# Performance work log

Measured on AMD Instinct MI355X. Metric: run time of the kernel, lower is better.

## Reference

```python
import jax, jax.numpy as jnp
import numpy as np

EMBED_DIM = 1024
HEADS = 16
HEAD_DIM = EMBED_DIM // HEADS
DIST_LAMBDA = -0.1
LN_EPS = 1e-5


def setup_inputs() -> dict:
    key = jax.random.key(0)
    ks = jax.random.split(key, 16)
    B, N, D = 32, 4096, EMBED_DIM
    s = 1.0 / np.sqrt(D)
    inp = {
        "query": jax.random.normal(ks[0], (B, D), jnp.float32),
        "context": jax.random.normal(ks[1], (B, N, D), jnp.float32),
        "dist_matrix": jax.random.uniform(ks[2], (B, 1, N), jnp.float32),
        "context_mask": jax.random.randint(ks[3], (B, N), 0, 2, jnp.int32),
        "Wq": jax.random.normal(ks[4], (D, D), jnp.float32) * s,
        "bq": jnp.zeros((D,), jnp.float32),
        "Wk": jax.random.normal(ks[5], (D, D), jnp.float32) * s,
        "bk": jnp.zeros((D,), jnp.float32),
        "Wv": jax.random.normal(ks[6], (D, D), jnp.float32) * s,
        "bv": jnp.zeros((D,), jnp.float32),
        "Wo": jax.random.normal(ks[7], (D, D), jnp.float32) * s,
        "bo": jnp.zeros((D,), jnp.float32),
        "ln_gamma": jnp.ones((D,), jnp.float32),
        "ln_beta": jnp.zeros((D,), jnp.float32),
    }
    return inp


def reference(query, context, dist_matrix, context_mask,
              Wq, bq, Wk, bk, Wv, bv, Wo, bo, ln_gamma, ln_beta):
    B, N, D = context.shape
    H, hd = HEADS, HEAD_DIM
    # projections
    q = (query @ Wq + bq).reshape(B, H, hd)            # [B,H,hd] (single query)
    k = (context @ Wk + bk).reshape(B, N, H, hd)       # [B,N,H,hd]
    v = (context @ Wv + bv).reshape(B, N, H, hd)
    # scores: [B,H,N]
    scores = jnp.einsum("bhd,bnhd->bhn", q, k) / np.sqrt(hd)
    # additive Manhattan-distance bias, broadcast over heads
    scores = scores + dist_matrix * DIST_LAMBDA        # dist_matrix [B,1,N]
    # mask
    scores = jnp.where(context_mask[:, None, :] == 0, -1e9, scores)
    attn = jax.nn.softmax(scores, axis=-1)             # [B,H,N]
    attn_out = jnp.einsum("bhn,bnhd->bhd", attn, v).reshape(B, D)
    output = attn_out @ Wo + bo
    x = query + output
    # LayerNorm
    mu = jnp.mean(x, axis=-1, keepdims=True)
    var = jnp.mean((x - mu) ** 2, axis=-1, keepdims=True)
    return (x - mu) * jax.lax.rsqrt(var + LN_EPS) * ln_gamma + ln_beta
```

## Files before the change

### kernel.cpp

```cpp
#include <hip/hip_runtime.h>
#include <hip/hip_bf16.h>
#include <math.h>

#define DDIM 1024
#define NH 16
#define HDIM 64
#define SCALE 0.125f
#define DLAM -0.1f
#define LNEPS 1e-5f
#define NS 16
#define CHW 16
#define BROW 256
#define CBSTR 1032

typedef short bf16x8 __attribute__((ext_vector_type(8)));
typedef float f32x4 __attribute__((ext_vector_type(4)));

__device__ inline unsigned short f2bf(float x) {
    return __builtin_bit_cast(unsigned short, __float2bfloat16(x));
}

__device__ inline void wg_barrier_lds() {
    asm volatile("s_waitcnt lgkmcnt(0)" ::: "memory");
    __builtin_amdgcn_s_barrier();
    __builtin_amdgcn_sched_barrier(0);
}

__global__ __launch_bounds__(512) void k_q(const float* __restrict__ query,
                                           const float* __restrict__ Wq,
                                           const float* __restrict__ bq,
                                           float* __restrict__ qout) {
    int b = blockIdx.x, c0 = blockIdx.y * 128;
    __shared__ float qs[DDIM];
    __shared__ float ps[512];
    int t = threadIdx.x;
    for (int i = t; i < DDIM; i += 512) qs[i] = query[b * DDIM + i];
    __syncthreads();
    int cl = t & 127;
    int col = c0 + cl;
    int d0 = (t >> 7) * 256;
    float acc = 0.f;
#pragma unroll 8
    for (int d = d0; d < d0 + 256; ++d)
        acc = fmaf(qs[d], Wq[(size_t)d * DDIM + col], acc);
    ps[t] = acc;
    __syncthreads();
    if (t < 128)
        qout[b * DDIM + col] = ps[t] + ps[t + 128] + ps[t + 256] + ps[t + 384] + bq[col];
}

__global__ __launch_bounds__(256) void k_qp(const float* __restrict__ qin,
                                            const float* __restrict__ Wk,
                                            unsigned short* __restrict__ qpb) {
    int dt = blockIdx.x, bg = blockIdx.y;
    __shared__ float qs[8][DDIM];
    for (int i = threadIdx.x; i < 8 * DDIM; i += 256)
        qs[i >> 10][i & 1023] =
            qin[(size_t)(bg * 8 + (i >> 10)) * DDIM + (i & 1023)];
    __syncthreads();
    int h = threadIdx.x & 15, dl = threadIdx.x >> 4;
    int d = dt * 16 + dl;
    const float* wr = Wk + (size_t)d * DDIM + h * HDIM;
    float acc[8] = {0.f, 0.f, 0.f, 0.f, 0.f, 0.f, 0.f, 0.f};
#pragma unroll
    for (int j = 0; j < HDIM; ++j) {
        float wv = wr[j];
#pragma unroll
        for (int bb = 0; bb < 8; ++bb)
            acc[bb] = fmaf(wv, qs[bb][h * HDIM + j], acc[bb]);
    }
#pragma unroll
    for (int bb = 0; bb < 8; ++bb)
        qpb[((size_t)((bg * 8 + bb) * NH + h)) * DDIM + d] = f2bf(acc[bb] * SCALE);
}

__global__ __launch_bounds__(512) void k_sb(const float* __restrict__ qin,
                                            const float* __restrict__ bk,
                                            float* __restrict__ sb) {
    int idx = threadIdx.x;
    int b = idx >> 4, h = idx & 15;
    float acc = 0.f;
#pragma unroll
    for (int j = 0; j < HDIM; ++j)
        acc = fmaf(bk[h * HDIM + j], qin[b * DDIM + h * HDIM + j], acc);
    sb[idx] = acc * SCALE;
}

__global__ __launch_bounds__(256, 2) void k_flash2(
    const float* __restrict__ ctx, const unsigned short* __restrict__ qpb,
    const float* __restrict__ sb, const float* __restrict__ dist,
    const int* __restrict__ mask, float* __restrict__ partA,
    float* __restrict__ partM, float* __restrict__ partL, int N) {
    __shared__ unsigned short cbuf[2][CHW][CBSTR];
    __shared__ float red[4][CHW][17];
    __shared__ float dls[BROW];

    int b = blockIdx.x, ns = blockIdx.y;
    int t = threadIdx.x, lane = t & 63, w = t >> 6;
    int m = lane & 15, g = lane >> 4;
    int nb0 = ns * BROW;
    const int NIT = BROW / CHW;

    {
        float dv = dist[(size_t)b * N + nb0 + t] * DLAM;
        dls[t] = mask[(size_t)b * N + nb0 + t] ? dv : -1e30f;
    }
    bf16x8 qf[8];
#pragma unroll
    for (int j = 0; j < 8; ++j)
        qf[j] = *reinterpret_cast<const bf16x8*>(
            qpb + ((size_t)(b * NH + m)) * DDIM + w * 256 + j * 32 + g * 8);
    float sbv = sb[b * NH + m];

    f32x4 acc[16];
#pragma unroll
    for (int td = 0; td < 16; ++td) acc[td] = (f32x4){0.f, 0.f, 0.f, 0.f};
    float m_run = -1e30f, l_run = 0.f;

    const float4* cb4 = reinterpret_cast<const float4*>(ctx) +
                        ((size_t)b * N + nb0) * (DDIM / 4);
    float4 inflight[16];

#define LOADC(c)                                                  \
    {                                                             \
        const float4* src = cb4 + (size_t)(c) * CHW * (DDIM / 4); \
        _Pragma("unroll") for (int i = 0; i < 16; ++i)            \
            inflight[i] = src[i * 256 + t];                       \
    }
#define LOAD4(qq, c)                                                  \
    {                                                                 \
        const float4* src = cb4 + (size_t)(c) * CHW * (DDIM / 4);     \
        _Pragma("unroll") for (int i = (qq) * 4; i < (qq) * 4 + 4; ++i) \
            inflight[i] = src[i * 256 + t];                           \
    }
#define WRITECB(buf)                                                         \
    {                                                                        \
        _Pragma("unroll") for (int i = 0; i < 16; ++i) {                     \
            float4 v = inflight[i];                                          \
            unsigned lo = (unsigned)f2bf(v.x) | ((unsigned)f2bf(v.y) << 16); \
            unsigned hi = (unsigned)f2bf(v.z) | ((unsigned)f2bf(v.w) << 16); \
            *reinterpret_cast<uint2*>(&cbuf[buf][i][t * 4]) =                \
                make_uint2(lo, hi);                                          \
        }                                                                    \
    }
#define WRITE4(qq, buf)                                                      \
    {                                                                        \
        _Pragma("unroll") for (int i = (qq) * 4; i < (qq) * 4 + 4; ++i) {    \
            float4 v = inflight[i];                                          \
            unsigned lo = (unsigned)f2bf(v.x) | ((unsigned)f2bf(v.y) << 16); \
            unsigned hi = (unsigned)f2bf(v.z) | ((unsigned)f2bf(v.w) << 16); \
            *reinterpret_cast<uint2*>(&cbuf[buf][i][t * 4]) =                \
                make_uint2(lo, hi);                                          \
        }                                                                    \
    }

    LOADC(0);
    WRITECB(0);
    LOADC(1);

    int dcol = lane & 15;
    for (int c = 0; c < NIT; ++c) {
        wg_barrier_lds();
        int buf = c & 1;
        if (c + 2 < NIT) {
#pragma unroll
            for (int q = 0; q < 4; ++q) {
                WRITE4(q, buf ^ 1);
                __builtin_amdgcn_sched_barrier(0);
                LOAD4(q, c + 2);
                __builtin_amdgcn_sched_barrier(0);
            }
        } else if (c + 1 < NIT) {
            WRITECB(buf ^ 1);
        }
        f32x4 cS = {0.f, 0.f, 0.f, 0.f};
#pragma unroll
        for (int j = 0; j < 8; ++j) {
            bf16x8 a = *reinterpret_cast<const bf16x8*>(
                &cbuf[buf][m][w * 256 + j * 32 + g * 8]);
            cS = __builtin_amdgcn_mfma_f32_16x16x32_bf16(a, qf[j], cS, 0, 0, 0);
        }
#pragma unroll
        for (int r = 0; r < 4; ++r) red[w][g * 4 + r][m] = cS[r];
        wg_barrier_lds();
        float S[4];
#pragma unroll
        for (int r = 0; r < 4; ++r) {
            int n = g * 4 + r;
            S[r] = red[0][n][m] + red[1][n][m] + red[2][n][m] + red[3][n][m] +
                   sbv + dls[c * CHW + n];
        }
        float cm = fmaxf(fmaxf(S[0], S[1]), fmaxf(S[2], S[3]));
        cm = fmaxf(cm, __shfl_xor(cm, 16, 64));
        cm = fmaxf(cm, __shfl_xor(cm, 32, 64));
        float mnew = fmaxf(m_run, cm);
        float f = __expf(m_run - mnew);
        float p[4];
        float ls = 0.f;
#pragma unroll
        for (int r = 0; r < 4; ++r) {
            p[r] = __expf(S[r] - mnew);
            ls += p[r];
        }
        ls += __shfl_xor(ls, 16, 64);
        ls += __shfl_xor(ls, 32, 64);
        l_run = l_run * f + ls;
        m_run = mnew;
        bf16x8 pa = (bf16x8){0, 0, 0, 0, 0, 0, 0, 0};
        pa[0] = (short)f2bf(p[0]);
        pa[1] = (short)f2bf(p[1]);
        pa[2] = (short)f2bf(p[2]);
        pa[3] = (short)f2bf(p[3]);
        float fr[4];
#pragma unroll
        for (int r = 0; r < 4; ++r) fr[r] = __shfl(f, (lane >> 4) * 4 + r, 64);
#pragma unroll
        for (int td = 0; td < 16; ++td) {
            acc[td][0] *= fr[0];
            acc[td][1] *= fr[1];
            acc[td][2] *= fr[2];
            acc[td][3] *= fr[3];
        }
#pragma unroll
        for (int td = 0; td < 16; ++td) {
            int dc = w * 256 + td * 16 + dcol;
            bf16x8 bb = (bf16x8){0, 0, 0, 0, 0, 0, 0, 0};
            bb[0] = (short)cbuf[buf][g * 4 + 0][dc];
            bb[1] = (short)cbuf[buf][g * 4 + 1][dc];
            bb[2] = (short)cbuf[buf][g * 4 + 2][dc];
            bb[3] = (short)cbuf[buf][g * 4 + 3][dc];
            acc[td] = __builtin_amdgcn_mfma_f32_16x16x32_bf16(pa, bb, acc[td], 0, 0, 0);
        }
    }

#pragma unroll
    for (int td = 0; td < 16; ++td) {
#pragma unroll
        for (int r = 0; r < 4; ++r) {
            int h = g * 4 + r;
            partA[((size_t)((b * NS + ns) * NH + h)) * DDIM + w * 256 + td * 16 +
                  dcol] = acc[td][r];
        }
    }
    if (t < NH) {
        partM[(b * NS + ns) * NH + t] = m_run;
        partL[(b * NS + ns) * NH + t] = l_run;
    }
#undef LOADC
#undef LOAD4
#undef WRITECB
#undef WRITE4
}

__global__ __launch_bounds__(256) void k_comb(const float* __restrict__ partA,
                                              const float* __restrict__ partM,
                                              const float* __restrict__ partL,
                                              float* __restrict__ ctxa) {
    int row = blockIdx.x;
    int b = row >> 4, h = row & 15;
    float M = -1e30f;
#pragma unroll
    for (int ns = 0; ns < NS; ++ns)
        M = fmaxf(M, partM[(b * NS + ns) * NH + h]);
    float denom = 0.f;
#pragma unroll
    for (int ns = 0; ns < NS; ++ns)
        denom = fmaf(__expf(partM[(b * NS + ns) * NH + h] - M),
                     partL[(b * NS + ns) * NH + h], denom);
    float inv = 1.f / denom;
    int d4 = threadIdx.x * 4;
    float4 a = make_float4(0.f, 0.f, 0.f, 0.f);
#pragma unroll 8
    for (int ns = 0; ns < NS; ++ns) {
        float wv = __expf(partM[(b * NS + ns) * NH + h] - M);
        float4 v = *reinterpret_cast<const float4*>(
            partA + ((size_t)((b * NS + ns) * NH + h)) * DDIM + d4);
        a.x = fmaf(wv, v.x, a.x);
        a.y = fmaf(wv, v.y, a.y);
        a.z = fmaf(wv, v.z, a.z);
        a.w = fmaf(wv, v.w, a.w);
    }
    float4 o = make_float4(a.x * inv, a.y * inv, a.z * inv, a.w * inv);
    *reinterpret_cast<float4*>(ctxa + (size_t)row * DDIM + d4) = o;
}

__global__ __launch_bounds__(256) void k_vproj(const float* __restrict__ ctxa,
                                               const float* __restrict__ Wv,
                                               const float* __restrict__ bv,
                                               float* __restrict__ oattn) {
    int b = blockIdx.x, c0 = blockIdx.y * 128;
    int h0 = c0 >> 6;
    __shared__ float cs[2][DDIM];
    __shared__ float ps[256];
    for (int i = threadIdx.x; i < 2 * DDIM; i += 256)
        cs[i >> 10][i & 1023] =
            ctxa[((size_t)(b * NH + h0 + (i >> 10))) * DDIM + (i & 1023)];
    __syncthreads();
    int t = threadIdx.x;
    int cl = t & 127;
    int col = c0 + cl;
    int hl = cl >> 6;
    int d0 = (t >> 7) * 512;
    float acc = 0.f;
#pragma unroll 8
    for (int d = d0; d < d0 + 512; ++d)
        acc = fmaf(cs[hl][d], Wv[(size_t)d * DDIM + col], acc);
    ps[t] = acc;
    __syncthreads();
    if (t < 128) oattn[b * DDIM + col] = ps[t] + ps[t + 128] + bv[col];
}

__global__ __launch_bounds__(256) void k_oproj(const float* __restrict__ query,
                                               const float* __restrict__ oattn,
                                               const float* __restrict__ Wo,
                                               const float* __restrict__ bo,
                                               float* __restrict__ x) {
    int b = blockIdx.x, c0 = blockIdx.y * 128;
    __shared__ float os[DDIM];
    __shared__ float ps[256];
    for (int i = threadIdx.x; i < DDIM; i += 256) os[i] = oattn[b * DDIM + i];
    __syncthreads();
    int t = threadIdx.x;
    int col = c0 + (t & 127);
    int d0 = (t >> 7) * 512;
    float acc = 0.f;
#pragma unroll 8
    for (int d = d0; d < d0 + 512; ++d)
        acc = fmaf(os[d], Wo[(size_t)d * DDIM + col], acc);
    ps[t] = acc;
    __syncthreads();
    if (t < 128)
        x[b * DDIM + col] = query[b * DDIM + col] + ps[t] + ps[t + 128] + bo[col];
}

__global__ __launch_bounds__(256) void k_ln(const float* __restrict__ x,
                                            const float* __restrict__ gamma,
                                            const float* __restrict__ beta,
                                            float* __restrict__ out) {
    int b = blockIdx.x;
    int t = threadIdx.x;
    __shared__ float red[8];
    float xv[4];
    float lsum = 0.f;
#pragma unroll
    for (int k = 0; k < 4; ++k) {
        xv[k] = x[b * DDIM + t + k * 256];
        lsum += xv[k];
    }
#pragma unroll
    for (int off = 32; off > 0; off >>= 1) lsum += __shfl_xor(lsum, off, 64);
    if ((t & 63) == 0) red[t >> 6] = lsum;
    __syncthreads();
    float mu = (red[0] + red[1] + red[2] + red[3]) * (1.f / DDIM);
    float lsq = 0.f;
#pragma unroll
    for (int k = 0; k < 4; ++k) {
        float dx = xv[k] - mu;
        lsq += dx * dx;
    }
#pragma unroll
    for (int off = 32; off > 0; off >>= 1) lsq += __shfl_xor(lsq, off, 64);
    if ((t & 63) == 0) red[4 + (t >> 6)] = lsq;
    __syncthreads();
    float var = (red[4] + red[5] + red[6] + red[7]) * (1.f / DDIM);
    float rstd = rsqrtf(var + LNEPS);
#pragma unroll
    for (int k = 0; k < 4; ++k) {
        int c = t + k * 256;
        out[b * DDIM + c] = (xv[k] - mu) * rstd * gamma[c] + beta[c];
    }
}

extern "C" void kernel_launch(void* const* d_in, const int* in_sizes, int n_in,
                              void* d_out, int out_size, void* d_ws, size_t ws_size,
                              hipStream_t stream) {
    const float* query = (const float*)d_in[0];
    const float* ctx   = (const float*)d_in[1];
    const float* dist  = (const float*)d_in[2];
    const int*   mask  = (const int*)d_in[3];
    const float* Wq = (const float*)d_in[4];
    const float* bq = (const float*)d_in[5];
    const float* Wk = (const float*)d_in[6];
    const float* bk = (const float*)d_in[7];
    const float* Wv = (const float*)d_in[8];
    const float* bv = (const float*)d_in[9];
    const float* Wo = (const float*)d_in[10];
    const float* bo = (const float*)d_in[11];
    const float* gamma = (const float*)d_in[12];
    const float* beta  = (const float*)d_in[13];
    float* out = (float*)d_out;

    int B = in_sizes[0] / DDIM;
    int N = in_sizes[1] / (B * DDIM);

    float* ws = (float*)d_ws;
    float* q = ws;
    unsigned short* qpb = (unsigned short*)(q + (size_t)B * DDIM);
    float* sb = (float*)(qpb + (size_t)B * NH * DDIM);
    float* partA = sb + (size_t)B * NH;
    float* partM = partA + (size_t)B * NS * NH * DDIM;
    float* partL = partM + (size_t)B * NS * NH;
    float* ctxa = partL + (size_t)B * NS * NH;
    float* oattn = ctxa + (size_t)B * NH * DDIM;
    float* xbuf = oattn + (size_t)B * DDIM;

    k_q<<<dim3(B, 8), 512, 0, stream>>>(query, Wq, bq, q);
    k_qp<<<dim3(DDIM / 16, B / 8), 256, 0, stream>>>(q, Wk, qpb);
    k_sb<<<1, B * NH, 0, stream>>>(q, bk, sb);
    k_flash2<<<dim3(B, NS), 256, 0, stream>>>(ctx, qpb, sb, dist, mask,
                                              partA, partM, partL, N);
    k_comb<<<B * NH, 256, 0, stream>>>(partA, partM, partL, ctxa);
    k_vproj<<<dim3(B, 8), 256, 0, stream>>>(ctxa, Wv, bv, oattn);
    k_oproj<<<dim3(B, 8), 256, 0, stream>>>(query, oattn, Wo, bo, xbuf);
    k_ln<<<B, 256, 0, stream>>>(xbuf, gamma, beta, out);
}
```

Before: 234.0 us.

## Fuse split-N combine into V projection, store partials as bf16, fold bias-score kernel

The per-split attention partials are now written in bf16 instead of fp32, halving that intermediate traffic. The separate combine kernel is removed: the V-projection kernel reweights and sums the partial accumulators for its two heads directly into shared memory. The tiny bias-score kernel is folded into the q-projection kernel, removing two launches in total. The trade-offs are bf16 rounding on the partial context vectors and redundant combine work, since each combine block recomputes the softmax weights.

```diff
diff --git a/kernel.cpp b/kernel.cpp
--- a/kernel.cpp
+++ b/kernel.cpp
@@ -19,6 +19,9 @@
 __device__ inline unsigned short f2bf(float x) {
     return __builtin_bit_cast(unsigned short, __float2bfloat16(x));
 }
+__device__ inline float bf2f(unsigned short u) {
+    return __builtin_bit_cast(float, (unsigned)u << 16);
+}
 
 __device__ inline void wg_barrier_lds() {
     asm volatile("s_waitcnt lgkmcnt(0)" ::: "memory");
@@ -51,13 +54,23 @@
 
 __global__ __launch_bounds__(256) void k_qp(const float* __restrict__ qin,
                                             const float* __restrict__ Wk,
-                                            unsigned short* __restrict__ qpb) {
+                                            const float* __restrict__ bk,
+                                            unsigned short* __restrict__ qpb,
+                                            float* __restrict__ sb) {
     int dt = blockIdx.x, bg = blockIdx.y;
     __shared__ float qs[8][DDIM];
     for (int i = threadIdx.x; i < 8 * DDIM; i += 256)
         qs[i >> 10][i & 1023] =
             qin[(size_t)(bg * 8 + (i >> 10)) * DDIM + (i & 1023)];
     __syncthreads();
+    if (dt == 0 && threadIdx.x < 128) {
+        int bb = threadIdx.x >> 4, h = threadIdx.x & 15;
+        float a = 0.f;
+#pragma unroll
+        for (int j = 0; j < HDIM; ++j)
+            a = fmaf(bk[h * HDIM + j], qs[bb][h * HDIM + j], a);
+        sb[(bg * 8 + bb) * NH + h] = a * SCALE;
+    }
     int h = threadIdx.x & 15, dl = threadIdx.x >> 4;
     int d = dt * 16 + dl;
     const float* wr = Wk + (size_t)d * DDIM + h * HDIM;
@@ -74,22 +87,10 @@
         qpb[((size_t)((bg * 8 + bb) * NH + h)) * DDIM + d] = f2bf(acc[bb] * SCALE);
 }
 
-__global__ __launch_bounds__(512) void k_sb(const float* __restrict__ qin,
-                                            const float* __restrict__ bk,
-                                            float* __restrict__ sb) {
-    int idx = threadIdx.x;
-    int b = idx >> 4, h = idx & 15;
-    float acc = 0.f;
-#pragma unroll
-    for (int j = 0; j < HDIM; ++j)
-        acc = fmaf(bk[h * HDIM + j], qin[b * DDIM + h * HDIM + j], acc);
-    sb[idx] = acc * SCALE;
-}
-
 __global__ __launch_bounds__(256, 2) void k_flash2(
     const float* __restrict__ ctx, const unsigned short* __restrict__ qpb,
     const float* __restrict__ sb, const float* __restrict__ dist,
-    const int* __restrict__ mask, float* __restrict__ partA,
+    const int* __restrict__ mask, unsigned short* __restrict__ partAb,
     float* __restrict__ partM, float* __restrict__ partL, int N) {
     __shared__ unsigned short cbuf[2][CHW][CBSTR];
     __shared__ float red[4][CHW][17];
@@ -238,8 +239,8 @@
 #pragma unroll
         for (int r = 0; r < 4; ++r) {
             int h = g * 4 + r;
-            partA[((size_t)((b * NS + ns) * NH + h)) * DDIM + w * 256 + td * 16 +
-                  dcol] = acc[td][r];
+            partAb[((size_t)((b * NS + ns) * NH + h)) * DDIM + w * 256 + td * 16 +
+                   dcol] = f2bf(acc[td][r]);
         }
     }
     if (t < NH) {
@@ -252,51 +253,46 @@
 #undef WRITE4
 }
 
-__global__ __launch_bounds__(256) void k_comb(const float* __restrict__ partA,
-                                              const float* __restrict__ partM,
-                                              const float* __restrict__ partL,
-                                              float* __restrict__ ctxa) {
-    int row = blockIdx.x;
-    int b = row >> 4, h = row & 15;
-    float M = -1e30f;
-#pragma unroll
-    for (int ns = 0; ns < NS; ++ns)
-        M = fmaxf(M, partM[(b * NS + ns) * NH + h]);
-    float denom = 0.f;
-#pragma unroll
-    for (int ns = 0; ns < NS; ++ns)
-        denom = fmaf(__expf(partM[(b * NS + ns) * NH + h] - M),
-                     partL[(b * NS + ns) * NH + h], denom);
-    float inv = 1.f / denom;
-    int d4 = threadIdx.x * 4;
-    float4 a = make_float4(0.f, 0.f, 0.f, 0.f);
-#pragma unroll 8
-    for (int ns = 0; ns < NS; ++ns) {
-        float wv = __expf(partM[(b * NS + ns) * NH + h] - M);
-        float4 v = *reinterpret_cast<const float4*>(
-            partA + ((size_t)((b * NS + ns) * NH + h)) * DDIM + d4);
-        a.x = fmaf(wv, v.x, a.x);
-        a.y = fmaf(wv, v.y, a.y);
-        a.z = fmaf(wv, v.z, a.z);
-        a.w = fmaf(wv, v.w, a.w);
-    }
-    float4 o = make_float4(a.x * inv, a.y * inv, a.z * inv, a.w * inv);
-    *reinterpret_cast<float4*>(ctxa + (size_t)row * DDIM + d4) = o;
-}
-
-__global__ __launch_bounds__(256) void k_vproj(const float* __restrict__ ctxa,
-                                               const float* __restrict__ Wv,
-                                               const float* __restrict__ bv,
-                                               float* __restrict__ oattn) {
+__global__ __launch_bounds__(256) void k_combv2(const unsigned short* __restrict__ partAb,
+                                                const float* __restrict__ partM,
+                                                const float* __restrict__ partL,
+                                                const float* __restrict__ Wv,
+                                                const float* __restrict__ bv,
+                                                float* __restrict__ oattn) {
     int b = blockIdx.x, c0 = blockIdx.y * 128;
     int h0 = c0 >> 6;
     __shared__ float cs[2][DDIM];
+    __shared__ float wn_s[2][NS];
     __shared__ float ps[256];
-    for (int i = threadIdx.x; i < 2 * DDIM; i += 256)
-        cs[i >> 10][i & 1023] =
-            ctxa[((size_t)(b * NH + h0 + (i >> 10))) * DDIM + (i & 1023)];
-    __syncthreads();
     int t = threadIdx.x;
+    if (t < 2) {
+        int h = h0 + t;
+        float M = -1e30f;
+#pragma unroll
+        for (int ns = 0; ns < NS; ++ns)
+            M = fmaxf(M, partM[(b * NS + ns) * NH + h]);
+        float den = 0.f;
+#pragma unroll
+        for (int ns = 0; ns < NS; ++ns)
+            den = fmaf(__expf(partM[(b * NS + ns) * NH + h] - M),
+                       partL[(b * NS + ns) * NH + h], den);
+        float inv = 1.f / den;
+#pragma unroll
+        for (int ns = 0; ns < NS; ++ns)
+            wn_s[t][ns] = __expf(partM[(b * NS + ns) * NH + h] - M) * inv;
+    }
+    __syncthreads();
+    for (int i = t; i < 2 * DDIM; i += 256) {
+        int hh = i >> 10, d = i & 1023;
+        float s = 0.f;
+#pragma unroll
+        for (int ns = 0; ns < NS; ++ns)
+            s = fmaf(wn_s[hh][ns],
+                     bf2f(partAb[((size_t)((b * NS + ns) * NH + h0 + hh)) * DDIM + d]),
+                     s);
+        cs[hh][d] = s;
+    }
+    __syncthreads();
     int cl = t & 127;
     int col = c0 + cl;
     int hl = cl >> 6;
@@ -397,20 +393,17 @@
     float* q = ws;
     unsigned short* qpb = (unsigned short*)(q + (size_t)B * DDIM);
     float* sb = (float*)(qpb + (size_t)B * NH * DDIM);
-    float* partA = sb + (size_t)B * NH;
-    float* partM = partA + (size_t)B * NS * NH * DDIM;
+    unsigned short* partAb = (unsigned short*)(sb + (size_t)B * NH);
+    float* partM = (float*)(partAb + (size_t)B * NS * NH * DDIM);
     float* partL = partM + (size_t)B * NS * NH;
-    float* ctxa = partL + (size_t)B * NS * NH;
-    float* oattn = ctxa + (size_t)B * NH * DDIM;
+    float* oattn = partL + (size_t)B * NS * NH;
     float* xbuf = oattn + (size_t)B * DDIM;
 
     k_q<<<dim3(B, 8), 512, 0, stream>>>(query, Wq, bq, q);
-    k_qp<<<dim3(DDIM / 16, B / 8), 256, 0, stream>>>(q, Wk, qpb);
-    k_sb<<<1, B * NH, 0, stream>>>(q, bk, sb);
+    k_qp<<<dim3(DDIM / 16, B / 8), 256, 0, stream>>>(q, Wk, bk, qpb, sb);
     k_flash2<<<dim3(B, NS), 256, 0, stream>>>(ctx, qpb, sb, dist, mask,
-                                              partA, partM, partL, N);
-    k_comb<<<B * NH, 256, 0, stream>>>(partA, partM, partL, ctxa);
-    k_vproj<<<dim3(B, 8), 256, 0, stream>>>(ctxa, Wv, bv, oattn);
+                                              partAb, partM, partL, N);
+    k_combv2<<<dim3(B, 8), 256, 0, stream>>>(partAb, partM, partL, Wv, bv, oattn);
     k_oproj<<<dim3(B, 8), 256, 0, stream>>>(query, oattn, Wo, bo, xbuf);
     k_ln<<<B, 256, 0, stream>>>(xbuf, gamma, beta, out);
 }
```

After: 215.8 us, median of 2. -7.8%, faster.
